# Optimization experiments

Measured on AMD Instinct MI355X. Metric: run time of the kernel, lower is better.

## Reference

```python
import jax, jax.numpy as jnp
import numpy as np

OUT_FEATURES = 11008
IN_FEATURES = 4096
GROUP_SIZE = 32
NUM_GROUPS = OUT_FEATURES * IN_FEATURES // GROUP_SIZE        # 1,409,024
NUM_PACKED = NUM_GROUPS * (GROUP_SIZE // 8 * 3)              # 16,908,288 bytes


def block_dequantize_3bit(weight_q3, weight_norm):
    """Unpack 3-bit codes (8 values per 3 bytes) and dequantize to fp32."""
    p = weight_q3.reshape(-1, 3).astype(jnp.int32)  # [N/8, 3] bytes
    b0, b1, b2 = p[:, 0], p[:, 1], p[:, 2]
    q = jnp.stack([
        b0 & 7,
        (b0 >> 3) & 7,
        ((b0 >> 6) & 3) | ((b1 & 1) << 2),
        (b1 >> 1) & 7,
        (b1 >> 4) & 7,
        ((b1 >> 7) & 1) | ((b2 & 3) << 1),
        (b2 >> 2) & 7,
        (b2 >> 5) & 7,
    ], axis=-1)                                     # [N/8, 8] codes in 0..7
    q = q.reshape(NUM_GROUPS, GROUP_SIZE).astype(jnp.float32)
    norm = weight_norm.astype(jnp.float32)[:, None]  # [num_groups, 1]
    w = (q / 7.0) * 2.0 * norm - norm                # map [0,7] -> [-norm, norm]
    return w.reshape(OUT_FEATURES, IN_FEATURES)


def setup_inputs() -> dict:
    key = jax.random.key(0)
    k1, k2, k3, k4 = jax.random.split(key, 4)
    x = jax.random.normal(k1, (4, 128, IN_FEATURES), dtype=jnp.float32)
    weight_q3 = jax.random.randint(k2, (NUM_PACKED,), 0, 256, dtype=jnp.int32)
    weight_norm = (jax.random.uniform(k3, (NUM_GROUPS,), dtype=jnp.float32) * 0.1 + 0.01).astype(jnp.float16)
    bias = jax.random.normal(k4, (OUT_FEATURES,), dtype=jnp.float32) * 0.02
    return {"x": x, "weight_q3": weight_q3, "weight_norm": weight_norm, "bias": bias}


def reference(x, weight_q3, weight_norm, bias):
    w = block_dequantize_3bit(weight_q3, weight_norm)  # [out, in] fp32
    return jnp.einsum('bsd,od->bso', x, w) + bias
```

## Files before the change

### kernel.cpp

```cpp
#include <hip/hip_runtime.h>
#include <hip/hip_fp16.h>

#define M_TOTAL 512
#define N_TOTAL 11008
#define K_TOTAL 4096
#define BM 128
#define BN 64
#define BK 64
#define NT (K_TOTAL / BK)
#define LDK 72

typedef short bf16x8 __attribute__((ext_vector_type(8)));
typedef float f32x4 __attribute__((ext_vector_type(4)));

__device__ __forceinline__ unsigned int pack2_bf16(float f0, float f1) {
    unsigned int u0 = __builtin_bit_cast(unsigned int, f0) + 0x8000u;
    unsigned int u1 = __builtin_bit_cast(unsigned int, f1) + 0x8000u;
    return (u0 >> 16) | (u1 & 0xFFFF0000u);
}

__device__ __forceinline__ void async_ld16(void* lds, const void* g) {
    __builtin_amdgcn_global_load_lds(
        (const __attribute__((address_space(1))) unsigned int*)g,
        (__attribute__((address_space(3))) unsigned int*)lds, 16, 0, 0);
}

__global__ void detect_norm_dtype(const void* __restrict__ wn, int* __restrict__ mode_out) {
    if (threadIdx.x != 0 || blockIdx.x != 0) return;
    const unsigned short* u16 = (const unsigned short*)wn;
    const float* f32p = (const float*)wn;
    bool ok_bf16 = true, ok_f16 = true, ok_f32 = true;
    for (int i = 0; i < 64; ++i) {
        float vb = __builtin_bit_cast(float, (unsigned int)u16[i] << 16);
        if (!(vb > 0.005f && vb < 0.12f)) ok_bf16 = false;
        float vh = __half2float(__builtin_bit_cast(__half, u16[i]));
        if (!(vh > 0.005f && vh < 0.12f)) ok_f16 = false;
        float vf = f32p[i];
        if (!(vf > 0.005f && vf < 0.12f)) ok_f32 = false;
    }
    *mode_out = ok_bf16 ? 2 : (ok_f16 ? 1 : 0);
}

__global__ void __launch_bounds__(256)
convert_x_kernel(const float* __restrict__ x, unsigned short* __restrict__ xb) {
    const int i = (blockIdx.x * 256 + threadIdx.x) * 4;
    const float4 v = *(const float4*)&x[i];
    *(uint2*)&xb[i] = make_uint2(pack2_bf16(v.x, v.y), pack2_bf16(v.z, v.w));
}

__global__ void __launch_bounds__(256)
l3b_gemm_pipe(const unsigned short* __restrict__ xb, const int* __restrict__ wq,
              const void* __restrict__ wnorm, const float* __restrict__ bias,
              float* __restrict__ out, const int* __restrict__ mode_ptr)
{
    __shared__ unsigned short As[2][BM * 64];
    __shared__ unsigned short Bs[2][BN * 64];

    const int mode = *mode_ptr;
    const int tid  = threadIdx.x;
    const int m0   = blockIdx.x * BM;
    const int n0   = blockIdx.y * BN;

    const int wid  = tid >> 6;
    const int lane = tid & 63;
    const int quad = lane >> 4;
    const int lm   = lane & 15;
    const int wm   = (wid >> 1) * 64;
    const int wn   = (wid & 1) * 32;

    const int arow0 = wid * 32 + (lane >> 3);
    const int acol  = ((lane & 7) ^ ((lane >> 3) & 7)) * 8;
    const int aslot = (lane & 7) * 8;

    const int gin      = tid >> 1;
    const int half     = tid & 1;
    const int bn_local = gin >> 1;
    const int bkg      = gin & 1;
    const int c0       = bkg * 4 + half * 2;
    const int swz      = bn_local & 7;

    auto stageA = [&](int it, int buf) {
#pragma unroll
        for (int j = 0; j < 4; ++j) {
            const int row = arow0 + j * 8;
            async_ld16(&As[buf][(row << 6) + aslot],
                       &xb[(size_t)(m0 + row) * K_TOTAL + it * 64 + acol]);
        }
    };

    int2 w0a, w1a, w2a; float na;
    int2 w0b, w1b, w2b; float nb;

    auto loadNorm = [&](int g) -> float {
        if (mode == 0)      return ((const float*)wnorm)[g];
        else if (mode == 1) return __half2float(((const __half*)wnorm)[g]);
        else                return __builtin_bit_cast(float,
                               (unsigned int)((const unsigned short*)wnorm)[g] << 16);
    };
    auto loadB = [&](int it, int2& w0, int2& w1, int2& w2, float& nrm) {
        const int g    = (n0 + bn_local) * (K_TOTAL / 32) + it * 2 + bkg;
        const int base = g * 12 + half * 6;
        w0 = *(const int2*)&wq[base];
        w1 = *(const int2*)&wq[base + 2];
        w2 = *(const int2*)&wq[base + 4];
        nrm = loadNorm(g);
    };
    auto decodeB = [&](int2 w0, int2 w1, int2 w2, float nrm, int buf) {
        const float a = nrm * (2.0f / 7.0f);
        const float b = -nrm;
        const unsigned int bits0 =
            (unsigned)w0.x | ((unsigned)w0.y << 8) | ((unsigned)w1.x << 16);
        const unsigned int bits1 =
            (unsigned)w1.y | ((unsigned)w2.x << 8) | ((unsigned)w2.y << 16);
        unsigned int packs[8];
#pragma unroll
        for (int t3 = 0; t3 < 2; ++t3) {
            const unsigned int bits = t3 ? bits1 : bits0;
#pragma unroll
            for (int j = 0; j < 4; ++j) {
                const float f0 = fmaf((float)((bits >> (6 * j)) & 7), a, b);
                const float f1 = fmaf((float)((bits >> (6 * j + 3)) & 7), a, b);
                packs[t3 * 4 + j] = pack2_bf16(f0, f1);
            }
        }
        *(uint4*)&Bs[buf][(bn_local << 6) + ((c0 ^ swz) << 3)] =
            make_uint4(packs[0], packs[1], packs[2], packs[3]);
        *(uint4*)&Bs[buf][(bn_local << 6) + (((c0 + 1) ^ swz) << 3)] =
            make_uint4(packs[4], packs[5], packs[6], packs[7]);
    };

    f32x4 acc[4][2];
#pragma unroll
    for (int i = 0; i < 4; ++i)
#pragma unroll
        for (int j = 0; j < 2; ++j) acc[i][j] = (f32x4){0.f, 0.f, 0.f, 0.f};

    auto mfmaTile = [&](const unsigned short* Asb, const unsigned short* Bsb) {
#pragma unroll
        for (int ks = 0; ks < 2; ++ks) {
            const int cswz = (((ks * 4 + quad) ^ (lm & 7)) << 3);
            bf16x8 aF[4], bF[2];
#pragma unroll
            for (int mi = 0; mi < 4; ++mi)
                aF[mi] = *(const bf16x8*)&Asb[((wm + mi * 16 + lm) << 6) + cswz];
#pragma unroll
            for (int ni = 0; ni < 2; ++ni)
                bF[ni] = *(const bf16x8*)&Bsb[((wn + ni * 16 + lm) << 6) + cswz];
#pragma unroll
            for (int mi = 0; mi < 4; ++mi)
#pragma unroll
                for (int ni = 0; ni < 2; ++ni)
                    acc[mi][ni] = __builtin_amdgcn_mfma_f32_16x16x32_bf16(
                        aF[mi], bF[ni], acc[mi][ni], 0, 0, 0);
        }
    };

    stageA(0, 0);
    loadB(0, w0a, w1a, w2a, na);
    decodeB(w0a, w1a, w2a, na, 0);
    loadB(1, w0b, w1b, w2b, nb);
    __syncthreads();

    for (int it = 0; it < NT; it += 2) {
        if (it + 1 < NT) {
            stageA(it + 1, 1);
            decodeB(w0b, w1b, w2b, nb, 1);
        }
        if (it + 2 < NT) loadB(it + 2, w0a, w1a, w2a, na);
        mfmaTile(As[0], Bs[0]);
        __syncthreads();

        if (it + 2 < NT) {
            stageA(it + 2, 0);
            decodeB(w0a, w1a, w2a, na, 0);
        }
        if (it + 3 < NT) loadB(it + 3, w0b, w1b, w2b, nb);
        mfmaTile(As[1], Bs[1]);
        __syncthreads();
    }

#pragma unroll
    for (int ni = 0; ni < 2; ++ni) {
        const int o  = n0 + wn + ni * 16 + lm;
        const float bv = bias[o];
#pragma unroll
        for (int mi = 0; mi < 4; ++mi) {
#pragma unroll
            for (int r = 0; r < 4; ++r) {
                const int m = m0 + wm + mi * 16 + quad * 4 + r;
                out[m * N_TOTAL + o] = acc[mi][ni][r] + bv;
            }
        }
    }
}

__global__ void __launch_bounds__(256)
l3b_gemm_kernel(const float* __restrict__ x, const int* __restrict__ wq,
                const void* __restrict__ wnorm, const float* __restrict__ bias,
                float* __restrict__ out, const int* __restrict__ mode_ptr)
{
    __shared__ unsigned short As[BM * LDK];
    __shared__ unsigned short Bs[BN * LDK];

    const int mode = *mode_ptr;
    const int tid  = threadIdx.x;
    const int m0   = blockIdx.y * BM;
    const int n0   = blockIdx.x * BN;
    const int wid  = tid >> 6;
    const int lane = tid & 63;
    const int quad = lane >> 4;
    const int lm   = lane & 15;
    const int wm   = (wid >> 1) * 64;
    const int wn   = (wid & 1) * 32;

    f32x4 acc[4][2];
#pragma unroll
    for (int i = 0; i < 4; ++i)
#pragma unroll
        for (int j = 0; j < 2; ++j) acc[i][j] = (f32x4){0.f, 0.f, 0.f, 0.f};

    const int ar = tid >> 4;
    const int ac = (tid & 15) * 4;
    const int gin      = tid >> 1;
    const int half     = tid & 1;
    const int bn_local = gin >> 1;
    const int bkg      = gin & 1;

    for (int it = 0; it < NT; ++it) {
        const int k0 = it * BK;
        __syncthreads();
#pragma unroll
        for (int p = 0; p < 8; ++p) {
            const int row = p * 16 + ar;
            const float4 v = *(const float4*)&x[(m0 + row) * K_TOTAL + k0 + ac];
            *(uint2*)&As[row * LDK + ac] =
                make_uint2(pack2_bf16(v.x, v.y), pack2_bf16(v.z, v.w));
        }
        {
            const int g    = (n0 + bn_local) * (K_TOTAL / 32) + it * 2 + bkg;
            const int base = g * 12 + half * 6;
            const int2 w0 = *(const int2*)&wq[base];
            const int2 w1 = *(const int2*)&wq[base + 2];
            const int2 w2 = *(const int2*)&wq[base + 4];
            float nrm;
            if (mode == 0)      nrm = ((const float*)wnorm)[g];
            else if (mode == 1) nrm = __half2float(((const __half*)wnorm)[g]);
            else                nrm = __builtin_bit_cast(float,
                                    (unsigned int)((const unsigned short*)wnorm)[g] << 16);
            const float a = nrm * (2.0f / 7.0f);
            const float b = -nrm;
            const unsigned int bits0 =
                (unsigned)w0.x | ((unsigned)w0.y << 8) | ((unsigned)w1.x << 16);
            const unsigned int bits1 =
                (unsigned)w1.y | ((unsigned)w2.x << 8) | ((unsigned)w2.y << 16);
            unsigned int packs[8];
#pragma unroll
            for (int t3 = 0; t3 < 2; ++t3) {
                const unsigned int bits = t3 ? bits1 : bits0;
#pragma unroll
                for (int j = 0; j < 4; ++j) {
                    const float f0 = fmaf((float)((bits >> (6 * j)) & 7), a, b);
                    const float f1 = fmaf((float)((bits >> (6 * j + 3)) & 7), a, b);
                    packs[t3 * 4 + j] = pack2_bf16(f0, f1);
                }
            }
            unsigned int* dst = (unsigned int*)&Bs[bn_local * LDK + bkg * 32 + half * 16];
            *(uint4*)dst       = make_uint4(packs[0], packs[1], packs[2], packs[3]);
            *(uint4*)(dst + 4) = make_uint4(packs[4], packs[5], packs[6], packs[7]);
        }
        __syncthreads();
#pragma unroll
        for (int ks = 0; ks < 2; ++ks) {
            const int kb = ks * 32 + quad * 8;
            bf16x8 aF[4], bF[2];
#pragma unroll
            for (int mi = 0; mi < 4; ++mi)
                aF[mi] = *(const bf16x8*)&As[(wm + mi * 16 + lm) * LDK + kb];
#pragma unroll
            for (int ni = 0; ni < 2; ++ni)
                bF[ni] = *(const bf16x8*)&Bs[(wn + ni * 16 + lm) * LDK + kb];
#pragma unroll
            for (int mi = 0; mi < 4; ++mi)
#pragma unroll
                for (int ni = 0; ni < 2; ++ni)
                    acc[mi][ni] = __builtin_amdgcn_mfma_f32_16x16x32_bf16(
                        aF[mi], bF[ni], acc[mi][ni], 0, 0, 0);
        }
    }
#pragma unroll
    for (int ni = 0; ni < 2; ++ni) {
        const int o  = n0 + wn + ni * 16 + lm;
        const float bv = bias[o];
#pragma unroll
        for (int mi = 0; mi < 4; ++mi)
#pragma unroll
            for (int r = 0; r < 4; ++r) {
                const int m = m0 + wm + mi * 16 + quad * 4 + r;
                out[m * N_TOTAL + o] = acc[mi][ni][r] + bv;
            }
    }
}

extern "C" void kernel_launch(void* const* d_in, const int* in_sizes, int n_in,
                              void* d_out, int out_size, void* d_ws, size_t ws_size,
                              hipStream_t stream) {
    const float* x    = (const float*)d_in[0];
    const int*   wq   = (const int*)d_in[1];
    const void*  wn   = d_in[2];
    const float* bias = (const float*)d_in[3];
    float* out = (float*)d_out;
    int* mode = (int*)d_ws;

    detect_norm_dtype<<<1, 64, 0, stream>>>(wn, mode);

    const size_t need = 256 + (size_t)M_TOTAL * K_TOTAL * 2;
    if (ws_size >= need) {
        unsigned short* xb = (unsigned short*)((char*)d_ws + 256);
        convert_x_kernel<<<(M_TOTAL * K_TOTAL / 4) / 256, 256, 0, stream>>>(x, xb);
        dim3 grid(M_TOTAL / BM, N_TOTAL / BN);
        l3b_gemm_pipe<<<grid, 256, 0, stream>>>(xb, wq, wn, bias, out, mode);
    } else {
        dim3 grid(N_TOTAL / BN, M_TOTAL / BM);
        l3b_gemm_kernel<<<grid, 256, 0, stream>>>(x, wq, wn, bias, out, mode);
    }
}
```

Before: 207.3 us.

## Halve M tile, remap blocks for XCD locality, reorder decode after loads

```diff
diff --git a/kernel.cpp b/kernel.cpp
--- a/kernel.cpp
+++ b/kernel.cpp
@@ -4,7 +4,7 @@
 #define M_TOTAL 512
 #define N_TOTAL 11008
 #define K_TOTAL 4096
-#define BM 128
+#define BM 64
 #define BN 64
 #define BK 64
 #define NT (K_TOTAL / BK)
@@ -26,19 +26,18 @@
 }
 
 __global__ void detect_norm_dtype(const void* __restrict__ wn, int* __restrict__ mode_out) {
-    if (threadIdx.x != 0 || blockIdx.x != 0) return;
+    const int i = threadIdx.x;
     const unsigned short* u16 = (const unsigned short*)wn;
     const float* f32p = (const float*)wn;
-    bool ok_bf16 = true, ok_f16 = true, ok_f32 = true;
-    for (int i = 0; i < 64; ++i) {
-        float vb = __builtin_bit_cast(float, (unsigned int)u16[i] << 16);
-        if (!(vb > 0.005f && vb < 0.12f)) ok_bf16 = false;
-        float vh = __half2float(__builtin_bit_cast(__half, u16[i]));
-        if (!(vh > 0.005f && vh < 0.12f)) ok_f16 = false;
-        float vf = f32p[i];
-        if (!(vf > 0.005f && vf < 0.12f)) ok_f32 = false;
-    }
-    *mode_out = ok_bf16 ? 2 : (ok_f16 ? 1 : 0);
+    const float vb = __builtin_bit_cast(float, (unsigned int)u16[i] << 16);
+    const float vh = __half2float(__builtin_bit_cast(__half, u16[i]));
+    const float vf = f32p[i];
+    const unsigned long long mb = __ballot(vb > 0.005f && vb < 0.12f);
+    const unsigned long long mh = __ballot(vh > 0.005f && vh < 0.12f);
+    const unsigned long long mf = __ballot(vf > 0.005f && vf < 0.12f);
+    if (i == 0)
+        *mode_out = (mb == ~0ull) ? 2 : ((mh == ~0ull) ? 1 : 0);
+    (void)mf;
 }
 
 __global__ void __launch_bounds__(256)
@@ -48,7 +47,7 @@
     *(uint2*)&xb[i] = make_uint2(pack2_bf16(v.x, v.y), pack2_bf16(v.z, v.w));
 }
 
-__global__ void __launch_bounds__(256)
+__global__ void __launch_bounds__(256, 5)
 l3b_gemm_pipe(const unsigned short* __restrict__ xb, const int* __restrict__ wq,
               const void* __restrict__ wnorm, const float* __restrict__ bias,
               float* __restrict__ out, const int* __restrict__ mode_ptr)
@@ -58,17 +57,20 @@
 
     const int mode = *mode_ptr;
     const int tid  = threadIdx.x;
-    const int m0   = blockIdx.x * BM;
-    const int n0   = blockIdx.y * BN;
+
+    const int bid = blockIdx.x;
+    const int w   = (bid & 7) * 172 + (bid >> 3);
+    const int m0  = (w & 7) * BM;
+    const int n0  = (w >> 3) * BN;
 
     const int wid  = tid >> 6;
     const int lane = tid & 63;
     const int quad = lane >> 4;
     const int lm   = lane & 15;
-    const int wm   = (wid >> 1) * 64;
+    const int wm   = (wid >> 1) * 32;
     const int wn   = (wid & 1) * 32;
 
-    const int arow0 = wid * 32 + (lane >> 3);
+    const int arow0 = wid * 8 + (lane >> 3);
     const int acol  = ((lane & 7) ^ ((lane >> 3) & 7)) * 8;
     const int aslot = (lane & 7) * 8;
 
@@ -81,8 +83,8 @@
 
     auto stageA = [&](int it, int buf) {
 #pragma unroll
-        for (int j = 0; j < 4; ++j) {
-            const int row = arow0 + j * 8;
+        for (int j = 0; j < 2; ++j) {
+            const int row = arow0 + j * 32;
             async_ld16(&As[buf][(row << 6) + aslot],
                        &xb[(size_t)(m0 + row) * K_TOTAL + it * 64 + acol]);
         }
@@ -129,9 +131,9 @@
             make_uint4(packs[4], packs[5], packs[6], packs[7]);
     };
 
-    f32x4 acc[4][2];
-#pragma unroll
-    for (int i = 0; i < 4; ++i)
+    f32x4 acc[2][2];
+#pragma unroll
+    for (int i = 0; i < 2; ++i)
 #pragma unroll
         for (int j = 0; j < 2; ++j) acc[i][j] = (f32x4){0.f, 0.f, 0.f, 0.f};
 
@@ -139,15 +141,15 @@
 #pragma unroll
         for (int ks = 0; ks < 2; ++ks) {
             const int cswz = (((ks * 4 + quad) ^ (lm & 7)) << 3);
-            bf16x8 aF[4], bF[2];
-#pragma unroll
-            for (int mi = 0; mi < 4; ++mi)
+            bf16x8 aF[2], bF[2];
+#pragma unroll
+            for (int mi = 0; mi < 2; ++mi)
                 aF[mi] = *(const bf16x8*)&Asb[((wm + mi * 16 + lm) << 6) + cswz];
 #pragma unroll
             for (int ni = 0; ni < 2; ++ni)
                 bF[ni] = *(const bf16x8*)&Bsb[((wn + ni * 16 + lm) << 6) + cswz];
 #pragma unroll
-            for (int mi = 0; mi < 4; ++mi)
+            for (int mi = 0; mi < 2; ++mi)
 #pragma unroll
                 for (int ni = 0; ni < 2; ++ni)
                     acc[mi][ni] = __builtin_amdgcn_mfma_f32_16x16x32_bf16(
@@ -162,19 +164,15 @@
     __syncthreads();
 
     for (int it = 0; it < NT; it += 2) {
-        if (it + 1 < NT) {
-            stageA(it + 1, 1);
-            decodeB(w0b, w1b, w2b, nb, 1);
-        }
+        if (it + 1 < NT) stageA(it + 1, 1);
         if (it + 2 < NT) loadB(it + 2, w0a, w1a, w2a, na);
+        if (it + 1 < NT) decodeB(w0b, w1b, w2b, nb, 1);
         mfmaTile(As[0], Bs[0]);
         __syncthreads();
 
-        if (it + 2 < NT) {
-            stageA(it + 2, 0);
-            decodeB(w0a, w1a, w2a, na, 0);
-        }
+        if (it + 2 < NT) stageA(it + 2, 0);
         if (it + 3 < NT) loadB(it + 3, w0b, w1b, w2b, nb);
+        if (it + 2 < NT) decodeB(w0a, w1a, w2a, na, 0);
         mfmaTile(As[1], Bs[1]);
         __syncthreads();
     }
@@ -184,7 +182,7 @@
         const int o  = n0 + wn + ni * 16 + lm;
         const float bv = bias[o];
 #pragma unroll
-        for (int mi = 0; mi < 4; ++mi) {
+        for (int mi = 0; mi < 2; ++mi) {
 #pragma unroll
             for (int r = 0; r < 4; ++r) {
                 const int m = m0 + wm + mi * 16 + quad * 4 + r;
@@ -199,13 +197,13 @@
                 const void* __restrict__ wnorm, const float* __restrict__ bias,
                 float* __restrict__ out, const int* __restrict__ mode_ptr)
 {
-    __shared__ unsigned short As[BM * LDK];
-    __shared__ unsigned short Bs[BN * LDK];
+    __shared__ unsigned short As[128 * LDK];
+    __shared__ unsigned short Bs[64 * LDK];
 
     const int mode = *mode_ptr;
     const int tid  = threadIdx.x;
-    const int m0   = blockIdx.y * BM;
-    const int n0   = blockIdx.x * BN;
+    const int m0   = blockIdx.y * 128;
+    const int n0   = blockIdx.x * 64;
     const int wid  = tid >> 6;
     const int lane = tid & 63;
     const int quad = lane >> 4;
@@ -317,10 +315,10 @@
     if (ws_size >= need) {
         unsigned short* xb = (unsigned short*)((char*)d_ws + 256);
         convert_x_kernel<<<(M_TOTAL * K_TOTAL / 4) / 256, 256, 0, stream>>>(x, xb);
-        dim3 grid(M_TOTAL / BM, N_TOTAL / BN);
-        l3b_gemm_pipe<<<grid, 256, 0, stream>>>(xb, wq, wn, bias, out, mode);
+        l3b_gemm_pipe<<<(M_TOTAL / BM) * (N_TOTAL / BN), 256, 0, stream>>>(
+            xb, wq, wn, bias, out, mode);
     } else {
-        dim3 grid(N_TOTAL / BN, M_TOTAL / BM);
+        dim3 grid(N_TOTAL / 64, M_TOTAL / 128);
         l3b_gemm_kernel<<<grid, 256, 0, stream>>>(x, wq, wn, bias, out, mode);
     }
 }
```

New measurement: 242.9 us. 17.1% more time.
